# Kernel tuning notes

Hardware: AMD Instinct MI355X
Metric: run time of the kernel (lower is better)

The kernel has to match this reference:

```python
import jax, jax.numpy as jnp
import numpy as np

NC = 80          # num classes (len(yolov8.names))
CONF = 0.25      # ultralytics conf_thres default
IOU_T = 0.45     # ultralytics iou_thres default
MAX_DET = 300    # module default max_det
K = 1024         # pre-NMS candidate cap (static stand-in for max_nms)
MAX_WH = 7680.0  # ultralytics class-offset for multi-class NMS


def setup_inputs() -> dict:
    key = jax.random.key(0)
    k1, k2, k3 = jax.random.split(key, 3)
    B, A = 32, 8400
    # YOLOv8 head layout: rows 0:4 = xywh (pixels), rows 4: = sigmoid class scores
    xy = jax.random.uniform(k1, (B, 2, A), dtype=jnp.float32) * 640.0
    wh = jax.random.uniform(k2, (B, 2, A), dtype=jnp.float32) * 160.0 + 8.0
    scores = jax.random.uniform(k3, (B, NC, A), dtype=jnp.float32) ** 3  # mostly below conf_thres
    preds = jnp.concatenate([xy, wh, scores], axis=1)  # [B, 4+NC, A]
    return {"preds": preds}


def _box_iou(b):
    # b: [K, 4] xyxy -> [K, K] pairwise IoU
    area = (b[:, 2] - b[:, 0]) * (b[:, 3] - b[:, 1])
    lt = jnp.maximum(b[:, None, :2], b[None, :, :2])
    rb = jnp.minimum(b[:, None, 2:], b[None, :, 2:])
    wh = jnp.clip(rb - lt, 0.0)
    inter = wh[..., 0] * wh[..., 1]
    return inter / (area[:, None] + area[None, :] - inter + 1e-7)


def _nms_single(pred):
    # pred: [4+NC, A]
    boxes_xywh = pred[:4].T           # [A, 4]
    cls_scores = pred[4:].T           # [A, NC]
    conf = cls_scores.max(-1)         # best-class confidence per anchor
    cls = jnp.argmax(cls_scores, -1)
    score = jnp.where(conf > CONF, conf, 0.0)
    top, idx = jax.lax.top_k(score, K)            # K candidates by confidence
    xywh = boxes_xywh[idx]
    half = xywh[:, 2:] * 0.5
    boxes = jnp.concatenate([xywh[:, :2] - half, xywh[:, :2] + half], -1)  # xyxy
    cls_k = cls[idx]
    valid = top > CONF
    # multi-class NMS via per-class coordinate offset (ultralytics trick)
    iou = _box_iou(boxes + (cls_k.astype(boxes.dtype) * MAX_WH)[:, None])
    ar = jnp.arange(K)

    def body(i, st):
        supp, keep = st
        ki = valid[i] & ~supp[i]
        keep = keep.at[i].set(ki)
        supp = supp | (ki & (iou[i] > IOU_T) & (ar > i))
        return supp, keep

    _, keep = jax.lax.fori_loop(0, K, body,
                                (jnp.zeros(K, bool), jnp.zeros(K, bool)))
    fscore = jnp.where(keep, top, 0.0)
    sc, order = jax.lax.top_k(fscore, MAX_DET)
    det = jnp.concatenate(
        [boxes[order], top[order][:, None], cls_k[order].astype(boxes.dtype)[:, None]], -1)
    # pad invalid rows with value NC in every column (matches F.pad(value=len(names)))
    return jnp.where((sc > CONF)[:, None], det, jnp.float32(NC))


def reference(preds):
    # [B, MAX_DET, 6] -> (x1, y1, x2, y2, conf, cls), padded rows filled with NC
    return jax.vmap(_nms_single)(preds)
```

## Files before the change

### kernel.cpp

```cpp
#include <hip/hip_runtime.h>
#include <stdint.h>

typedef unsigned long long u64;
typedef unsigned int u32;

#define NC 80
#define CONF_T 0.25f
#define IOU_THR 0.45f
#define MAX_DET 300
#define KBIG 1024
#define A_ANCH 8400
#define NROWS 84
#define MAX_WH 7680.0f
#define HBINS 256
#define BIN_BASE 0x3e80u

__device__ __forceinline__ void hadd(u32* h, u32 bin, bool m, int lane) {
    u64 act = __ballot(m);
    if (act == 0) return;
    int fl = __ffsll((unsigned long long)act) - 1;
    u32 fb = __shfl(bin, fl);
    u64 same = __ballot(m && (bin == fb));
    if (lane == fl) atomicAdd(&h[fb], (u32)__popcll(same));
    if (m && (bin != fb)) atomicAdd(&h[bin], 1u);
}

__global__ __launch_bounds__(512) void yolo_conf_kernel(const float* __restrict__ preds,
                                                        u64* __restrict__ keys,
                                                        u32* __restrict__ hist) {
    int b = blockIdx.x / 9;
    int slab = blockIdx.x % 9;
    if (slab == 0 && threadIdx.x < HBINS) hist[(size_t)b * HBINS + threadIdx.x] = 0;
    int g = slab * 512 + threadIdx.x;
    if (g >= A_ANCH / 2) return;
    int a0 = g * 2;
    const float* base = preds + ((size_t)b * NROWS + 4) * A_ANCH + a0;
    float2 best = *(const float2*)base;
    int bc0 = 0, bc1 = 0;
#pragma unroll 8
    for (int c = 1; c < NC; ++c) {
        float2 v = *(const float2*)(base + (size_t)c * A_ANCH);
        if (v.x > best.x) { best.x = v.x; bc0 = c; }
        if (v.y > best.y) { best.y = v.y; bc1 = c; }
    }
    float s0 = (best.x > CONF_T) ? best.x : 0.0f;
    float s1 = (best.y > CONF_T) ? best.y : 0.0f;
    ulonglong2 kk;
    kk.x = ((u64)__float_as_uint(s0) << 32) | ((u64)(16383 - a0) << 7) | (u64)bc0;
    kk.y = ((u64)__float_as_uint(s1) << 32) | ((u64)(16383 - (a0 + 1)) << 7) | (u64)bc1;
    *(ulonglong2*)(keys + (size_t)b * A_ANCH + a0) = kk;
}

__global__ __launch_bounds__(256) void yolo_prep_kernel(const float* __restrict__ preds,
                                                        const u64* __restrict__ keys,
                                                        float4* __restrict__ obox,
                                                        float4* __restrict__ pbox,
                                                        u32* __restrict__ hist) {
    __shared__ u32 lh[HBINS];
    const int lane = threadIdx.x & 63;
    int b = blockIdx.x / 33;
    int a = (blockIdx.x % 33) * 256 + threadIdx.x;
    lh[threadIdx.x] = 0;
    __syncthreads();

    u32 bits = 0, bin = 0;
    bool act = a < A_ANCH;
    if (act) {
        u64 key = keys[(size_t)b * A_ANCH + a];
        bits = (u32)(key >> 32);
        int cls = (int)(key & 127u);
        const float* pb = preds + (size_t)b * NROWS * A_ANCH + a;
        float x = pb[0];
        float y = pb[A_ANCH];
        float w = pb[2 * A_ANCH];
        float h = pb[3 * A_ANCH];
        float hw = __fmul_rn(w, 0.5f), hh = __fmul_rn(h, 0.5f);
        float x1 = __fsub_rn(x, hw), x2 = __fadd_rn(x, hw);
        float y1 = __fsub_rn(y, hh), y2 = __fadd_rn(y, hh);
        float4 pB; pB.x = x1; pB.y = y1; pB.z = x2; pB.w = y2;
        pbox[(size_t)b * A_ANCH + a] = pB;
        float off = __fmul_rn((float)cls, MAX_WH);
        float4 oB;
        oB.x = __fadd_rn(x1, off); oB.y = __fadd_rn(y1, off);
        oB.z = __fadd_rn(x2, off); oB.w = __fadd_rn(y2, off);
        obox[(size_t)b * A_ANCH + a] = oB;
        bin = (bits >> 16) - BIN_BASE;
        if (bin > 255u) bin = 255u;
    }
    hadd(lh, bin, act && (bits != 0u), lane);
    __syncthreads();
    u32 c = lh[threadIdx.x];
    if (c) atomicAdd(&hist[(size_t)b * HBINS + threadIdx.x], c);
}

__device__ __forceinline__ float iou_f(float ix1, float iy1, float ix2, float iy2, float iar,
                                       float jx1, float jy1, float jx2, float jy2, float jar) {
    float lx = fmaxf(ix1, jx1), ly = fmaxf(iy1, jy1);
    float rx = fminf(ix2, jx2), ry = fminf(iy2, jy2);
    float ww = fmaxf(__fsub_rn(rx, lx), 0.0f);
    float hh = fmaxf(__fsub_rn(ry, ly), 0.0f);
    float inter = __fmul_rn(ww, hh);
    float den = __fadd_rn(__fsub_rn(__fadd_rn(iar, jar), inter), 1e-7f);
    return __fdiv_rn(inter, den);
}

__device__ __forceinline__ u64 bstep(u64 v, u32 idx, u32 size, u32 stride) {
    u64 v2 = __shfl_xor((unsigned long long)v, (int)stride, 64);
    bool keep_big = (((idx & stride) == 0) == ((idx & size) == 0));
    return ((v > v2) == keep_big) ? v : v2;
}

__device__ __forceinline__ void radix_scan(u32* hist, int nb, int shift, u32* s_scal,
                                           u32* wsum, int tid, int lane, int wid) {
    int per = nb >> 10; if (per == 0) per = 1;
    int na = nb / per;
    u32 rem = s_scal[1];
    u32 Pk = s_scal[0];
    int hi = nb - 1 - per * tid;
    u32 s = 0;
    if (tid < na)
        for (int q = 0; q < per; ++q) s += hist[hi - q];
    u32 pre = s;
#pragma unroll
    for (int off = 1; off < 64; off <<= 1) {
        u32 o = __shfl_up(pre, off);
        if (lane >= off) pre += o;
    }
    if (lane == 63) wsum[wid] = pre;
    __syncthreads();
    u32 base = 0;
    for (int w = 0; w < wid; ++w) base += wsum[w];
    u32 run = base + pre - s;
    if (tid < na) {
        for (int q = 0; q < per; ++q) {
            int d = hi - q;
            u32 g = hist[d];
            if (run < rem && rem <= run + g) {
                s_scal[0] = Pk | ((u32)d << shift);
                s_scal[1] = rem - run;
            }
            run += g;
        }
    }
    __syncthreads();
}

union U2 {
    u32 hist[4096];
    struct { u32 eqw[264]; u32 wpre[264]; } tie;
};

__global__ __launch_bounds__(1024) void yolo_nms_kernel(const u64* __restrict__ keys,
                                                        const float4* __restrict__ obox,
                                                        const float4* __restrict__ pbox,
                                                        const u32* __restrict__ hist,
                                                        float* __restrict__ out) {
    const int b = blockIdx.x;
    const int tid = threadIdx.x;
    const int lane = tid & 63;
    const int wid = tid >> 6;

    __shared__ U2 u2;
    __shared__ u64 skey[KBIG];
    __shared__ float BX1[KBIG], BY1[KBIG], BX2[KBIG], BY2[KBIG], BAR[KBIG];
    __shared__ int keptlist[364];
    __shared__ float kx1[364], ky1[364], kx2[364], ky2[364], kar[364];
    __shared__ u32 kcls[364];
    __shared__ u64 rows[64];
    __shared__ u32 wsum[16];
    __shared__ u32 s_scal[4];
    __shared__ u32 s_cnt;
    __shared__ u32 s_csupp[2];
    __shared__ u32 s_nkept;

    const u64* kb = keys + (size_t)b * A_ANCH;

    u32 vals[9];
#pragma unroll
    for (int it = 0; it < 9; ++it) {
        int a = tid + it * 1024;
        vals[it] = (a < A_ANCH) ? (u32)(kb[a] >> 32) : 0u;
    }

    const u32* hb = hist + (size_t)b * HBINS;
    {
        u32 g = (tid < HBINS) ? hb[HBINS - 1 - tid] : 0u;
        u32 pre = g;
#pragma unroll
        for (int off = 1; off < 64; off <<= 1) {
            u32 o = __shfl_up(pre, off);
            if (lane >= off) pre += o;
        }
        if (lane == 63) wsum[wid] = pre;
        __syncthreads();
        u32 base = 0;
        for (int w = 0; w < wid; ++w) base += wsum[w];
        pre += base;
        u32 run = pre - g;
        if (tid < HBINS) {
            if (run < 512u && 512u <= pre) { s_scal[0] = (u32)(HBINS - 1 - tid); s_scal[2] = pre; }
            if (tid == HBINS - 1) {
                s_scal[3] = pre;
                if (pre < 512u) { s_scal[0] = 0; s_scal[2] = pre; }
            }
        }
        __syncthreads();
    }
    const u32 Pbin16 = BIN_BASE + s_scal[0];
    const u32 Cfast = s_scal[2];
    const u32 validN = s_scal[3];

    for (int pass = 0; pass < 2; ++pass) {
        u32 Ccand;
        if (pass == 0) {
            if (Cfast > (u32)KBIG) continue;
            Ccand = Cfast;
            skey[tid] = 0;
            if (tid == 0) { s_cnt = 0; s_nkept = 0; s_csupp[0] = 0; s_csupp[1] = 0; }
            __syncthreads();
#pragma unroll
            for (int it = 0; it < 9; ++it) {
                int a = tid + it * 1024;
                u32 v = vals[it];
                bool take = (a < A_ANCH) && (v != 0u) && ((v >> 16) >= Pbin16);
                u64 m = __ballot(take);
                if (m) {
                    int fl = __ffsll((unsigned long long)m) - 1;
                    u32 basep = 0;
                    if (lane == fl) basep = atomicAdd(&s_cnt, (u32)__popcll(m));
                    basep = __shfl(basep, fl);
                    if (take) {
                        u32 pos = basep + (u32)__popcll(m & ((1ull << lane) - 1ull));
                        if (pos < (u32)KBIG) skey[pos] = kb[a];
                    }
                }
            }
            __syncthreads();
        } else {
            for (int i = tid; i < 4096; i += 1024) u2.hist[i] = 0;
            if (tid == 0) {
                s_scal[0] = 0; s_scal[1] = (u32)KBIG; s_scal[2] = 0;
                s_nkept = 0; s_csupp[0] = 0; s_csupp[1] = 0;
            }
            __syncthreads();
#pragma unroll
            for (int it = 0; it < 9; ++it) {
                int a = tid + it * 1024;
                hadd(u2.hist, vals[it] >> 20, a < A_ANCH, lane);
            }
            __syncthreads();
            radix_scan(u2.hist, 4096, 20, s_scal, wsum, tid, lane, wid);
            for (int i = tid; i < 4096; i += 1024) u2.hist[i] = 0;
            __syncthreads();
            u32 Pk = s_scal[0];
#pragma unroll
            for (int it = 0; it < 9; ++it) {
                int a = tid + it * 1024;
                u32 v = vals[it];
                bool m = (a < A_ANCH) && ((v & 0xFFF00000u) == Pk);
                hadd(u2.hist, (v >> 8) & 4095u, m, lane);
            }
            __syncthreads();
            radix_scan(u2.hist, 4096, 8, s_scal, wsum, tid, lane, wid);
            for (int i = tid; i < 256; i += 1024) u2.hist[i] = 0;
            __syncthreads();
            Pk = s_scal[0];
#pragma unroll
            for (int it = 0; it < 9; ++it) {
                int a = tid + it * 1024;
                u32 v = vals[it];
                bool m = (a < A_ANCH) && ((v & 0xFFFFFF00u) == Pk);
                hadd(u2.hist, v & 255u, m, lane);
            }
            __syncthreads();
            radix_scan(u2.hist, 256, 0, s_scal, wsum, tid, lane, wid);
            const u32 P = s_scal[0];
            const u32 tEq = s_scal[1];
            if (tid < 264) u2.tie.eqw[tid] = 0;
            __syncthreads();
#pragma unroll
            for (int it = 0; it < 9; ++it) {
                int a = tid + it * 1024;
                if (a < A_ANCH && vals[it] == P) atomicOr(&u2.tie.eqw[a >> 5], 1u << (a & 31));
            }
            __syncthreads();
            if (wid == 0) {
                u32 cw[5], loc = 0;
#pragma unroll
                for (int q = 0; q < 5; ++q) {
                    int w2 = lane * 5 + q;
                    u32 e = (w2 < 264) ? u2.tie.eqw[w2] : 0u;
                    cw[q] = (u32)__popc(e); loc += cw[q];
                }
                u32 pre = loc;
#pragma unroll
                for (int off = 1; off < 64; off <<= 1) {
                    u32 o = __shfl_up(pre, off);
                    if (lane >= off) pre += o;
                }
                u32 run = pre - loc;
#pragma unroll
                for (int q = 0; q < 5; ++q) {
                    int w2 = lane * 5 + q;
                    if (w2 < 264) u2.tie.wpre[w2] = run;
                    run += cw[q];
                }
            }
            __syncthreads();
#pragma unroll
            for (int it = 0; it < 9; ++it) {
                int a = tid + it * 1024;
                bool take = false;
                if (a < A_ANCH) {
                    u32 v = vals[it];
                    take = v > P;
                    if (!take && v == P) {
                        u32 r = u2.tie.wpre[a >> 5] +
                                (u32)__popc(u2.tie.eqw[a >> 5] & ((1u << (a & 31)) - 1u));
                        take = (r < tEq);
                    }
                }
                u64 m = __ballot(take);
                if (m) {
                    int fl = __ffsll((unsigned long long)m) - 1;
                    u32 basep = 0;
                    if (lane == fl) basep = atomicAdd(&s_scal[2], (u32)__popcll(m));
                    basep = __shfl(basep, fl);
                    if (take) {
                        u32 pos = basep + (u32)__popcll(m & ((1ull << lane) - 1ull));
                        if (pos < (u32)KBIG) skey[pos] = kb[a];
                    }
                }
            }
            __syncthreads();
            Ccand = KBIG;
        }

        {
            u64 v = skey[tid];
#pragma unroll
            for (u32 size = 2; size <= 64; size <<= 1)
#pragma unroll
                for (u32 stride = size >> 1; stride >= 1; stride >>= 1)
                    v = bstep(v, (u32)tid, size, stride);
            for (u32 size = 128; size <= 1024; size <<= 1) {
                for (u32 stride = size >> 1; stride >= 64; stride >>= 1) {
                    skey[tid] = v;
                    __syncthreads();
                    u64 v2 = skey[tid ^ stride];
                    bool keep_big = ((((u32)tid & stride) == 0) == (((u32)tid & size) == 0));
                    v = ((v > v2) == keep_big) ? v : v2;
                    __syncthreads();
                }
#pragma unroll
                for (u32 stride = 32; stride >= 1; stride >>= 1)
                    v = bstep(v, (u32)tid, size, stride);
            }
            skey[tid] = v;
            __syncthreads();
        }

        {
            u64 key = skey[tid];
            int idx = 16383 - (int)((key >> 7) & 16383u);
            if (idx >= A_ANCH || idx < 0) idx = 0;
            float4 ob = obox[(size_t)b * A_ANCH + idx];
            BX1[tid] = ob.x; BY1[tid] = ob.y; BX2[tid] = ob.z; BY2[tid] = ob.w;
            BAR[tid] = __fmul_rn(__fsub_rn(ob.z, ob.x), __fsub_rn(ob.w, ob.y));
        }
        __syncthreads();

        const int nchunks = (int)((Ccand + 63u) >> 6);
        for (int c = 0; c < nchunks; ++c) {
            int j = c * 64 + lane;
            u64 keyj = skey[j];
            float scj = __uint_as_float((u32)(keyj >> 32));
            u32 clsj = (u32)(keyj & 127u);
            float jx1 = BX1[j], jy1 = BY1[j], jx2 = BX2[j], jy2 = BY2[j], jar = BAR[j];

            u32 nk = s_nkept;
            bool suppbit = false;
            for (u32 k = wid; k < nk; k += 16) {
                bool cm = (kcls[k] == clsj);
                if (__ballot(cm)) {
                    float iou = iou_f(kx1[k], ky1[k], kx2[k], ky2[k], kar[k],
                                      jx1, jy1, jx2, jy2, jar);
                    suppbit |= (cm && (iou > IOU_THR));
                }
            }
            u64 bm = __ballot(suppbit);
            if (bm && lane == 0) {
                atomicOr(&s_csupp[0], (u32)bm);
                atomicOr(&s_csupp[1], (u32)(bm >> 32));
            }
#pragma unroll
            for (int p2 = 0; p2 < 4; ++p2) {
                int i = p2 * 16 + wid;
                int ci = c * 64 + i;
                u32 clsi = (u32)(skey[ci] & 127u);
                u64 m = 0;
                if (__ballot(clsi == clsj)) {
                    float iou = iou_f(BX1[ci], BY1[ci], BX2[ci], BY2[ci], BAR[ci],
                                      jx1, jy1, jx2, jy2, jar);
                    m = __ballot((lane > i) && (iou > IOU_THR));
                }
                if (lane == 0) rows[i] = m;
            }
            __syncthreads();
            if (wid == 0) {
                u64 row = rows[lane];
                u32 rlo = (u32)row, rhi = (u32)(row >> 32);
                u64 csupp = (((u64)s_csupp[1]) << 32) | (u64)s_csupp[0];
                u64 validm = __ballot(scj > CONF_T) & ~csupp;
                u64 supp = 0, keep = 0;
#pragma unroll
                for (int i = 0; i < 64; ++i) {
                    u64 ri = (((u64)(u32)__builtin_amdgcn_readlane((int)rhi, i)) << 32) |
                             (u64)(u32)__builtin_amdgcn_readlane((int)rlo, i);
                    bool ki = (((validm & ~supp) >> i) & 1ull) != 0;
                    if (ki) { keep |= (1ull << i); supp |= ri; }
                }
                u32 basek = s_nkept;
                if ((keep >> lane) & 1ull) {
                    u32 slot = basek + (u32)__popcll(keep & ((1ull << lane) - 1ull));
                    keptlist[slot] = j;
                    kx1[slot] = jx1; ky1[slot] = jy1;
                    kx2[slot] = jx2; ky2[slot] = jy2;
                    kar[slot] = jar; kcls[slot] = clsj;
                }
                if (lane == 0) {
                    s_nkept = basek + (u32)__popcll(keep);
                    s_csupp[0] = 0; s_csupp[1] = 0;
                }
            }
            __syncthreads();
            if (s_nkept >= MAX_DET) break;
        }

        u32 nk = s_nkept;
        bool finished = (nk >= MAX_DET) || (Ccand >= validN) || (pass == 1);
        if (!finished) continue;

        if (tid < MAX_DET) {
            float row[6];
            int t = (tid < (int)(nk < MAX_DET ? nk : MAX_DET)) ? keptlist[tid] : -1;
            if (t >= 0) {
                u64 key = skey[t];
                float score = __uint_as_float((u32)(key >> 32));
                int cls = (int)(key & 127u);
                int idx = 16383 - (int)((key >> 7) & 16383u);
                if (idx >= A_ANCH || idx < 0) idx = 0;
                float4 pB = pbox[(size_t)b * A_ANCH + idx];
                row[0] = pB.x; row[1] = pB.y; row[2] = pB.z; row[3] = pB.w;
                row[4] = score;
                row[5] = (float)cls;
            } else {
                row[0] = row[1] = row[2] = row[3] = row[4] = row[5] = (float)NC;
            }
            float* o = out + ((size_t)b * MAX_DET + tid) * 6;
#pragma unroll
            for (int q = 0; q < 6; ++q) o[q] = row[q];
        }
        break;
    }
}

extern "C" void kernel_launch(void* const* d_in, const int* in_sizes, int n_in,
                              void* d_out, int out_size, void* d_ws, size_t ws_size,
                              hipStream_t stream) {
    const float* preds = (const float*)d_in[0];
    float* out = (float*)d_out;
    int B = in_sizes[0] / (NROWS * A_ANCH);
    u64* keys = (u64*)d_ws;
    float4* obox = (float4*)(keys + (size_t)B * A_ANCH);
    float4* pbox = obox + (size_t)B * A_ANCH;
    u32* hist = (u32*)(pbox + (size_t)B * A_ANCH);
    yolo_conf_kernel<<<dim3(B * 9), dim3(512), 0, stream>>>(preds, keys, hist);
    yolo_prep_kernel<<<dim3(B * 33), dim3(256), 0, stream>>>(preds, keys, obox, pbox, hist);
    yolo_nms_kernel<<<dim3(B), dim3(1024), 0, stream>>>(keys, obox, pbox, hist, out);
}
```

Baseline: 69.16 us.

## Drop pbox buffer, halve NMS block to 512 threads with two elements per thread

Removes the plain-box workspace buffer written by the prep kernel and instead recomputes the xyxy boxes from preds for the final 300 output rows. The NMS kernel now runs 512 threads per block, each handling two sort and gather elements. The shared-memory bitonic stages for strides of 64 and up are rewritten as in-place compare-exchange on pairs, and the per-wave loops are re-strided for 8 waves. This cuts global write traffic and synchronisation width, but leaves fewer waves for the serial NMS sweep.

New measurement: 73.59 us. 6.4% more time.

```diff
diff --git a/kernel.cpp b/kernel.cpp
--- a/kernel.cpp
+++ b/kernel.cpp
@@ -54,7 +54,6 @@
 __global__ __launch_bounds__(256) void yolo_prep_kernel(const float* __restrict__ preds,
                                                         const u64* __restrict__ keys,
                                                         float4* __restrict__ obox,
-                                                        float4* __restrict__ pbox,
                                                         u32* __restrict__ hist) {
     __shared__ u32 lh[HBINS];
     const int lane = threadIdx.x & 63;
@@ -77,8 +76,6 @@
         float hw = __fmul_rn(w, 0.5f), hh = __fmul_rn(h, 0.5f);
         float x1 = __fsub_rn(x, hw), x2 = __fadd_rn(x, hw);
         float y1 = __fsub_rn(y, hh), y2 = __fadd_rn(y, hh);
-        float4 pB; pB.x = x1; pB.y = y1; pB.z = x2; pB.w = y2;
-        pbox[(size_t)b * A_ANCH + a] = pB;
         float off = __fmul_rn((float)cls, MAX_WH);
         float4 oB;
         oB.x = __fadd_rn(x1, off); oB.y = __fadd_rn(y1, off);
@@ -112,7 +109,7 @@
 
 __device__ __forceinline__ void radix_scan(u32* hist, int nb, int shift, u32* s_scal,
                                            u32* wsum, int tid, int lane, int wid) {
-    int per = nb >> 10; if (per == 0) per = 1;
+    int per = nb >> 9; if (per == 0) per = 1;
     int na = nb / per;
     u32 rem = s_scal[1];
     u32 Pk = s_scal[0];
@@ -150,11 +147,11 @@
     struct { u32 eqw[264]; u32 wpre[264]; } tie;
 };
 
-__global__ __launch_bounds__(1024) void yolo_nms_kernel(const u64* __restrict__ keys,
-                                                        const float4* __restrict__ obox,
-                                                        const float4* __restrict__ pbox,
-                                                        const u32* __restrict__ hist,
-                                                        float* __restrict__ out) {
+__global__ __launch_bounds__(512) void yolo_nms_kernel(const float* __restrict__ preds,
+                                                       const u64* __restrict__ keys,
+                                                       const float4* __restrict__ obox,
+                                                       const u32* __restrict__ hist,
+                                                       float* __restrict__ out) {
     const int b = blockIdx.x;
     const int tid = threadIdx.x;
     const int lane = tid & 63;
@@ -167,25 +164,26 @@
     __shared__ float kx1[364], ky1[364], kx2[364], ky2[364], kar[364];
     __shared__ u32 kcls[364];
     __shared__ u64 rows[64];
-    __shared__ u32 wsum[16];
+    __shared__ u32 wsum[8];
     __shared__ u32 s_scal[4];
     __shared__ u32 s_cnt;
     __shared__ u32 s_csupp[2];
     __shared__ u32 s_nkept;
 
     const u64* kb = keys + (size_t)b * A_ANCH;
-
-    u32 vals[9];
-#pragma unroll
-    for (int it = 0; it < 9; ++it) {
-        int a = tid + it * 1024;
+    const u32* hb = hist + (size_t)b * HBINS;
+
+    u32 hg = (tid < HBINS) ? hb[HBINS - 1 - tid] : 0u;
+
+    u32 vals[17];
+#pragma unroll
+    for (int it = 0; it < 17; ++it) {
+        int a = tid + it * 512;
         vals[it] = (a < A_ANCH) ? (u32)(kb[a] >> 32) : 0u;
     }
 
-    const u32* hb = hist + (size_t)b * HBINS;
     {
-        u32 g = (tid < HBINS) ? hb[HBINS - 1 - tid] : 0u;
-        u32 pre = g;
+        u32 pre = hg;
 #pragma unroll
         for (int off = 1; off < 64; off <<= 1) {
             u32 o = __shfl_up(pre, off);
@@ -196,7 +194,7 @@
         u32 base = 0;
         for (int w = 0; w < wid; ++w) base += wsum[w];
         pre += base;
-        u32 run = pre - g;
+        u32 run = pre - hg;
         if (tid < HBINS) {
             if (run < 512u && 512u <= pre) { s_scal[0] = (u32)(HBINS - 1 - tid); s_scal[2] = pre; }
             if (tid == HBINS - 1) {
@@ -215,12 +213,12 @@
         if (pass == 0) {
             if (Cfast > (u32)KBIG) continue;
             Ccand = Cfast;
-            skey[tid] = 0;
+            skey[tid] = 0; skey[tid + 512] = 0;
             if (tid == 0) { s_cnt = 0; s_nkept = 0; s_csupp[0] = 0; s_csupp[1] = 0; }
             __syncthreads();
 #pragma unroll
-            for (int it = 0; it < 9; ++it) {
-                int a = tid + it * 1024;
+            for (int it = 0; it < 17; ++it) {
+                int a = tid + it * 512;
                 u32 v = vals[it];
                 bool take = (a < A_ANCH) && (v != 0u) && ((v >> 16) >= Pbin16);
                 u64 m = __ballot(take);
@@ -237,37 +235,37 @@
             }
             __syncthreads();
         } else {
-            for (int i = tid; i < 4096; i += 1024) u2.hist[i] = 0;
+            for (int i = tid; i < 4096; i += 512) u2.hist[i] = 0;
             if (tid == 0) {
                 s_scal[0] = 0; s_scal[1] = (u32)KBIG; s_scal[2] = 0;
                 s_nkept = 0; s_csupp[0] = 0; s_csupp[1] = 0;
             }
             __syncthreads();
 #pragma unroll
-            for (int it = 0; it < 9; ++it) {
-                int a = tid + it * 1024;
+            for (int it = 0; it < 17; ++it) {
+                int a = tid + it * 512;
                 hadd(u2.hist, vals[it] >> 20, a < A_ANCH, lane);
             }
             __syncthreads();
             radix_scan(u2.hist, 4096, 20, s_scal, wsum, tid, lane, wid);
-            for (int i = tid; i < 4096; i += 1024) u2.hist[i] = 0;
+            for (int i = tid; i < 4096; i += 512) u2.hist[i] = 0;
             __syncthreads();
             u32 Pk = s_scal[0];
 #pragma unroll
-            for (int it = 0; it < 9; ++it) {
-                int a = tid + it * 1024;
+            for (int it = 0; it < 17; ++it) {
+                int a = tid + it * 512;
                 u32 v = vals[it];
                 bool m = (a < A_ANCH) && ((v & 0xFFF00000u) == Pk);
                 hadd(u2.hist, (v >> 8) & 4095u, m, lane);
             }
             __syncthreads();
             radix_scan(u2.hist, 4096, 8, s_scal, wsum, tid, lane, wid);
-            for (int i = tid; i < 256; i += 1024) u2.hist[i] = 0;
+            for (int i = tid; i < 256; i += 512) u2.hist[i] = 0;
             __syncthreads();
             Pk = s_scal[0];
 #pragma unroll
-            for (int it = 0; it < 9; ++it) {
-                int a = tid + it * 1024;
+            for (int it = 0; it < 17; ++it) {
+                int a = tid + it * 512;
                 u32 v = vals[it];
                 bool m = (a < A_ANCH) && ((v & 0xFFFFFF00u) == Pk);
                 hadd(u2.hist, v & 255u, m, lane);
@@ -279,8 +277,8 @@
             if (tid < 264) u2.tie.eqw[tid] = 0;
             __syncthreads();
 #pragma unroll
-            for (int it = 0; it < 9; ++it) {
-                int a = tid + it * 1024;
+            for (int it = 0; it < 17; ++it) {
+                int a = tid + it * 512;
                 if (a < A_ANCH && vals[it] == P) atomicOr(&u2.tie.eqw[a >> 5], 1u << (a & 31));
             }
             __syncthreads();
@@ -308,8 +306,8 @@
             }
             __syncthreads();
 #pragma unroll
-            for (int it = 0; it < 9; ++it) {
-                int a = tid + it * 1024;
+            for (int it = 0; it < 17; ++it) {
+                int a = tid + it * 512;
                 bool take = false;
                 if (a < A_ANCH) {
                     u32 v = vals[it];
@@ -337,36 +335,46 @@
         }
 
         {
-            u64 v = skey[tid];
+            u64 vA = skey[tid], vB = skey[tid + 512];
+            const u32 iA = (u32)tid, iB = (u32)tid + 512;
 #pragma unroll
             for (u32 size = 2; size <= 64; size <<= 1)
 #pragma unroll
-                for (u32 stride = size >> 1; stride >= 1; stride >>= 1)
-                    v = bstep(v, (u32)tid, size, stride);
+                for (u32 stride = size >> 1; stride >= 1; stride >>= 1) {
+                    vA = bstep(vA, iA, size, stride);
+                    vB = bstep(vB, iB, size, stride);
+                }
+            skey[tid] = vA; skey[tid + 512] = vB;
+            __syncthreads();
             for (u32 size = 128; size <= 1024; size <<= 1) {
                 for (u32 stride = size >> 1; stride >= 64; stride >>= 1) {
-                    skey[tid] = v;
+                    u32 i1 = ((tid & ~(int)(stride - 1)) << 1) | (tid & (stride - 1));
+                    u32 i2 = i1 + stride;
+                    bool desc = ((i1 & size) == 0);
+                    u64 x = skey[i1], y = skey[i2];
+                    if ((x < y) == desc) { skey[i1] = y; skey[i2] = x; }
                     __syncthreads();
-                    u64 v2 = skey[tid ^ stride];
-                    bool keep_big = ((((u32)tid & stride) == 0) == (((u32)tid & size) == 0));
-                    v = ((v > v2) == keep_big) ? v : v2;
-                    __syncthreads();
-                }
-#pragma unroll
-                for (u32 stride = 32; stride >= 1; stride >>= 1)
-                    v = bstep(v, (u32)tid, size, stride);
-            }
-            skey[tid] = v;
-            __syncthreads();
-        }
-
-        {
-            u64 key = skey[tid];
+                }
+                vA = skey[tid]; vB = skey[tid + 512];
+#pragma unroll
+                for (u32 stride = 32; stride >= 1; stride >>= 1) {
+                    vA = bstep(vA, iA, size, stride);
+                    vB = bstep(vB, iB, size, stride);
+                }
+                skey[tid] = vA; skey[tid + 512] = vB;
+                __syncthreads();
+            }
+        }
+
+#pragma unroll
+        for (int q = 0; q < 2; ++q) {
+            int t = tid + q * 512;
+            u64 key = skey[t];
             int idx = 16383 - (int)((key >> 7) & 16383u);
             if (idx >= A_ANCH || idx < 0) idx = 0;
             float4 ob = obox[(size_t)b * A_ANCH + idx];
-            BX1[tid] = ob.x; BY1[tid] = ob.y; BX2[tid] = ob.z; BY2[tid] = ob.w;
-            BAR[tid] = __fmul_rn(__fsub_rn(ob.z, ob.x), __fsub_rn(ob.w, ob.y));
+            BX1[t] = ob.x; BY1[t] = ob.y; BX2[t] = ob.z; BY2[t] = ob.w;
+            BAR[t] = __fmul_rn(__fsub_rn(ob.z, ob.x), __fsub_rn(ob.w, ob.y));
         }
         __syncthreads();
 
@@ -380,7 +388,7 @@
 
             u32 nk = s_nkept;
             bool suppbit = false;
-            for (u32 k = wid; k < nk; k += 16) {
+            for (u32 k = wid; k < nk; k += 8) {
                 bool cm = (kcls[k] == clsj);
                 if (__ballot(cm)) {
                     float iou = iou_f(kx1[k], ky1[k], kx2[k], ky2[k], kar[k],
@@ -393,9 +401,10 @@
                 atomicOr(&s_csupp[0], (u32)bm);
                 atomicOr(&s_csupp[1], (u32)(bm >> 32));
             }
-#pragma unroll
-            for (int p2 = 0; p2 < 4; ++p2) {
-                int i = p2 * 16 + wid;
+
+#pragma unroll
+            for (int p2 = 0; p2 < 8; ++p2) {
+                int i = p2 * 8 + wid;
                 int ci = c * 64 + i;
                 u32 clsi = (u32)(skey[ci] & 127u);
                 u64 m = 0;
@@ -407,6 +416,7 @@
                 if (lane == 0) rows[i] = m;
             }
             __syncthreads();
+
             if (wid == 0) {
                 u64 row = rows[lane];
                 u32 rlo = (u32)row, rhi = (u32)(row >> 32);
@@ -450,8 +460,13 @@
                 int cls = (int)(key & 127u);
                 int idx = 16383 - (int)((key >> 7) & 16383u);
                 if (idx >= A_ANCH || idx < 0) idx = 0;
-                float4 pB = pbox[(size_t)b * A_ANCH + idx];
-                row[0] = pB.x; row[1] = pB.y; row[2] = pB.z; row[3] = pB.w;
+                const float* pb = preds + (size_t)b * NROWS * A_ANCH + idx;
+                float x = pb[0], y = pb[A_ANCH], w = pb[2 * A_ANCH], h = pb[3 * A_ANCH];
+                float hw = __fmul_rn(w, 0.5f), hh = __fmul_rn(h, 0.5f);
+                row[0] = __fsub_rn(x, hw);
+                row[1] = __fsub_rn(y, hh);
+                row[2] = __fadd_rn(x, hw);
+                row[3] = __fadd_rn(y, hh);
                 row[4] = score;
                 row[5] = (float)cls;
             } else {
@@ -473,9 +488,8 @@
     int B = in_sizes[0] / (NROWS * A_ANCH);
     u64* keys = (u64*)d_ws;
     float4* obox = (float4*)(keys + (size_t)B * A_ANCH);
-    float4* pbox = obox + (size_t)B * A_ANCH;
-    u32* hist = (u32*)(pbox + (size_t)B * A_ANCH);
+    u32* hist = (u32*)(obox + (size_t)B * A_ANCH);
     yolo_conf_kernel<<<dim3(B * 9), dim3(512), 0, stream>>>(preds, keys, hist);
-    yolo_prep_kernel<<<dim3(B * 33), dim3(256), 0, stream>>>(preds, keys, obox, pbox, hist);
-    yolo_nms_kernel<<<dim3(B), dim3(1024), 0, stream>>>(keys, obox, pbox, hist, out);
-}
+    yolo_prep_kernel<<<dim3(B * 33), dim3(256), 0, stream>>>(preds, keys, obox, hist);
+    yolo_nms_kernel<<<dim3(B), dim3(512), 0, stream>>>(preds, keys, obox, hist, out);
+}
```
